# Kernel tuning notes

Measured on AMD Instinct MI355X. Metric: run time of the kernel, lower is better.

The kernel has to match this reference:

```python
import jax, jax.numpy as jnp
import numpy as np

N = 8192
F_IN = 256
F_OUT = 256
S = 128          # state_dim
D_INNER = 512    # int(2.0 * out_features)


def _ln(x, g, b, eps=1e-5):
    m = x.mean(-1, keepdims=True)
    v = ((x - m) ** 2).mean(-1, keepdims=True)
    return (x - m) / jnp.sqrt(v + eps) * g + b


def setup_inputs() -> dict:
    key = jax.random.key(0)
    ks = jax.random.split(key, 20)
    s = 0.05
    d = {}
    d['h'] = jax.random.normal(ks[0], (N, F_IN), dtype=jnp.float32)
    d['adj'] = jax.random.randint(ks[1], (N, N), 0, 2, dtype=jnp.int32)
    d['W'] = jax.random.normal(ks[2], (F_IN, F_OUT), dtype=jnp.float32) * s
    d['a_src'] = jax.random.normal(ks[3], (F_OUT, 1), dtype=jnp.float32) * s
    d['a_dst'] = jax.random.normal(ks[4], (F_OUT, 1), dtype=jnp.float32) * s
    d['W_bcdt'] = jax.random.normal(ks[5], (F_OUT, 3 * S), dtype=jnp.float32) * s
    d['b_bcdt'] = jnp.zeros((3 * S,), jnp.float32)
    d['abp_w'] = jax.random.normal(ks[6], (S, F_OUT), dtype=jnp.float32) * s
    d['abp_b'] = jnp.zeros((F_OUT,), jnp.float32)
    d['cp_w'] = jax.random.normal(ks[7], (S, 1), dtype=jnp.float32) * s
    d['cp_b'] = jnp.zeros((1,), jnp.float32)
    d['W_hz'] = jax.random.normal(ks[8], (F_OUT, 2 * D_INNER), dtype=jnp.float32) * s
    d['b_hz'] = jnp.zeros((2 * D_INNER,), jnp.float32)
    d['out_w'] = jax.random.normal(ks[9], (D_INNER, F_OUT), dtype=jnp.float32) * s
    d['out_b'] = jnp.zeros((F_OUT,), jnp.float32)
    d['fe1_w'] = jax.random.normal(ks[10], (F_OUT, D_INNER), dtype=jnp.float32) * s
    d['fe1_b'] = jnp.zeros((D_INNER,), jnp.float32)
    d['fe_ln_g'] = jnp.ones((D_INNER,), jnp.float32)
    d['fe_ln_b'] = jnp.zeros((D_INNER,), jnp.float32)
    d['fe2_w'] = jax.random.normal(ks[11], (D_INNER, F_OUT), dtype=jnp.float32) * s
    d['fe2_b'] = jnp.zeros((F_OUT,), jnp.float32)
    d['A'] = jax.random.uniform(ks[12], (S,), minval=1.0, maxval=64.0, dtype=jnp.float32)
    d['D'] = jnp.ones((1,), jnp.float32)
    d['g1_w'] = jax.random.normal(ks[13], (2 * F_OUT, 2 * F_OUT), dtype=jnp.float32) * s
    d['g1_b'] = jnp.zeros((2 * F_OUT,), jnp.float32)
    d['g_ln_g'] = jnp.ones((2 * F_OUT,), jnp.float32)
    d['g_ln_b'] = jnp.zeros((2 * F_OUT,), jnp.float32)
    d['g2_w'] = jax.random.normal(ks[14], (2 * F_OUT, F_OUT), dtype=jnp.float32) * s
    d['g2_b'] = jnp.zeros((F_OUT,), jnp.float32)
    d['ln_g'] = jnp.ones((F_OUT,), jnp.float32)
    d['ln_b'] = jnp.zeros((F_OUT,), jnp.float32)
    return d


def reference(h, adj, W, a_src, a_dst, W_bcdt, b_bcdt, abp_w, abp_b, cp_w, cp_b,
              W_hz, b_hz, out_w, out_b, fe1_w, fe1_b, fe_ln_g, fe_ln_b, fe2_w,
              fe2_b, A, D, g1_w, g1_b, g_ln_g, g_ln_b, g2_w, g2_b, ln_g, ln_b):
    Wh = h @ W                                   # [N, F_OUT]
    # GAT-style masked attention
    e = Wh @ a_src + (Wh @ a_dst).T              # [N, N]
    e = jnp.where(e > 0, e, 0.2 * e)             # leaky_relu(0.2)
    e = jnp.where(adj > 0, e, jnp.float32(-9e15))
    attn = jax.nn.softmax(e, axis=1)
    h_attn = attn @ Wh                           # [N, F_OUT]
    # feature enhancer
    h_enh = jax.nn.silu(_ln(Wh @ fe1_w + fe1_b, fe_ln_g, fe_ln_b)) @ fe2_w + fe2_b
    # SSM-like branch
    BCdt = Wh @ W_bcdt + b_bcdt                  # [N, 3S]
    B, C, dt = jnp.split(BCdt, 3, axis=1)
    Asm = jax.nn.softmax(dt + A[None, :], axis=1)
    ab = (Asm * B) @ abp_w + abp_b               # [N, F_OUT]
    hs = Wh * ab
    hz = hs @ W_hz + b_hz                        # [N, 2*D_INNER]
    h_part, z = jnp.split(hz, 2, axis=1)
    hs = (h_part * jax.nn.silu(z) + h_part * D) @ out_w + out_b
    c_proj = C @ cp_w + cp_b                     # [N, 1]
    hs = hs * (1.0 + c_proj)
    # gated fusion
    comb = jnp.concatenate([h_attn, hs], axis=1)  # [N, 2*F_OUT]
    g = jax.nn.sigmoid(jax.nn.silu(_ln(comb @ g1_w + g1_b, g_ln_g, g_ln_b)) @ g2_w + g2_b)
    fused = g * h_attn + (1.0 - g) * hs + h_enh
    return _ln(fused, ln_g, ln_b)
```

## Files before the change

### kernel.cpp

```cpp
#include <hip/hip_runtime.h>
#include <cstdint>

typedef __attribute__((ext_vector_type(8))) short short8;
typedef __attribute__((ext_vector_type(4))) float f32x4;

#define DEVINL static __device__ __forceinline__

DEVINL ushort f2b(float f) {
    uint32_t u = __builtin_bit_cast(uint32_t, f);
    u += 0x7FFFu + ((u >> 16) & 1u);
    return (ushort)(u >> 16);
}

typedef __attribute__((address_space(3))) uint32_t lds_u32;
typedef const __attribute__((address_space(1))) uint32_t glb_u32;

DEVINL void load_lds_16(const ushort* g, ushort* l) {
    __builtin_amdgcn_global_load_lds((glb_u32*)g, (lds_u32*)l, 16, 0, 0);
}

constexpr int EPI_F32      = 0;
constexpr int EPI_MUL_BF16 = 2;
constexpr int EPI_SCALE_FB = 3;
constexpr int EPI_WH       = 4;

template<int K, int EPI>
__global__ __launch_bounds__(256) void gemm_k(
    const ushort* __restrict__ A, const ushort* __restrict__ BT,
    const float* __restrict__ bias, int N,
    float* __restrict__ outf, ushort* __restrict__ outb, int obld, int oboff,
    const float* __restrict__ extra,
    const float* __restrict__ asrc, const float* __restrict__ adst,
    float* __restrict__ sOut, float* __restrict__ dOut)
{
    __shared__ ushort Asm[64 * 64];
    __shared__ ushort Bsm[64 * 64];

    const int wave = threadIdx.x >> 6;
    const int lane = threadIdx.x & 63;
    const int quad = lane >> 4, l16 = lane & 15;
    const int lr = lane >> 3, ls = lane & 7;
    const int m0 = blockIdx.x * 64;
    const int n0 = blockIdx.y * 64;

    f32x4 zero = {0.f, 0.f, 0.f, 0.f};
    f32x4 acc[4] = {zero, zero, zero, zero};

    for (int k0 = 0; k0 < K; k0 += 64) {
        #pragma unroll
        for (int p = 0; p < 2; ++p) {
            const int r = wave * 16 + p * 8 + lr;
            load_lds_16(A + (size_t)(m0 + r) * K + k0 + ((ls ^ (r & 7)) * 8),
                        Asm + (size_t)(wave * 16 + p * 8) * 64);
            load_lds_16(BT + (size_t)(n0 + r) * K + k0 + ((ls ^ (r & 7)) * 8),
                        Bsm + (size_t)(wave * 16 + p * 8) * 64);
        }
        __syncthreads();
        #pragma unroll
        for (int ks = 0; ks < 2; ++ks) {
            const int sl = ((ks * 4 + quad) ^ (l16 & 7)) * 8;
            short8 af = *(const short8*)(Asm + (wave * 16 + l16) * 64 + sl);
            #pragma unroll
            for (int c = 0; c < 4; ++c) {
                short8 bf = *(const short8*)(Bsm + (c * 16 + l16) * 64 + sl);
                acc[c] = __builtin_amdgcn_mfma_f32_16x16x32_bf16(af, bf, acc[c], 0, 0, 0);
            }
        }
        __syncthreads();
    }

    #pragma unroll
    for (int r = 0; r < 4; ++r) {
        const int row = m0 + wave * 16 + quad * 4 + r;
        float sp = 0.f, dp = 0.f;
        #pragma unroll
        for (int c = 0; c < 4; ++c) {
            const int col = n0 + c * 16 + l16;
            float v = acc[c][r] + (bias ? bias[col] : 0.f);
            if (EPI == EPI_MUL_BF16) v *= extra[(size_t)row * N + col];
            if (EPI == EPI_SCALE_FB) v *= extra[row];
            if (EPI == EPI_F32 || EPI == EPI_SCALE_FB || EPI == EPI_WH)
                outf[(size_t)row * N + col] = v;
            if (EPI == EPI_MUL_BF16 || EPI == EPI_SCALE_FB || EPI == EPI_WH)
                outb[(size_t)row * obld + oboff + col] = f2b(v);
            if (EPI == EPI_WH) { sp += v * asrc[col]; dp += v * adst[col]; }
        }
        if (EPI == EPI_WH) {
            #pragma unroll
            for (int o = 1; o < 16; o <<= 1) {
                sp += __shfl_xor(sp, o);
                dp += __shfl_xor(dp, o);
            }
            if (l16 == 0) {
                atomicAdd(&sOut[row], sp);
                atomicAdd(&dOut[row], dp);
            }
        }
    }
}

constexpr int EPR_LNSILU = 0;
constexpr int EPR_BCDT   = 1;
constexpr int EPR_HZ     = 2;
constexpr int EPR_FINAL  = 3;

template<int K, int N, int EPI>
__global__ __launch_bounds__(256) void gemm_row(
    const ushort* __restrict__ A, const ushort* __restrict__ BT,
    const float* __restrict__ bias,
    float* __restrict__ outf, ushort* __restrict__ outb,
    const float* __restrict__ q0, const float* __restrict__ q1,
    const float* __restrict__ q2, const float* __restrict__ q3,
    const float* __restrict__ q4)
{
    constexpr int NW = N / 4;
    constexpr int NF = NW / 16;
    __shared__ ushort Asm[16 * 64];
    __shared__ ushort Bsm[N * 64];
    __shared__ float red[192];

    const int wave = threadIdx.x >> 6;
    const int lane = threadIdx.x & 63;
    const int quad = lane >> 4, l16 = lane & 15;
    const int lr = lane >> 3, ls = lane & 7;
    const int m0 = blockIdx.x * 16;
    const ushort* Bb = BT + (EPI == EPR_HZ ? (size_t)blockIdx.y * 512 * K : 0);

    f32x4 zero = {0.f, 0.f, 0.f, 0.f};
    f32x4 acc[NF];
    #pragma unroll
    for (int c = 0; c < NF; ++c) acc[c] = zero;

    for (int k0 = 0; k0 < K; k0 += 64) {
        if (wave < 2) {
            const int r = wave * 8 + lr;
            load_lds_16(A + (size_t)(m0 + r) * K + k0 + ((ls ^ (r & 7)) * 8),
                        Asm + (size_t)(wave * 8) * 64);
        }
        #pragma unroll
        for (int p = 0; p < NW / 8; ++p) {
            const int n = wave * NW + p * 8 + lr;
            load_lds_16(Bb + (size_t)n * K + k0 + ((ls ^ (n & 7)) * 8),
                        Bsm + (size_t)(wave * NW + p * 8) * 64);
        }
        __syncthreads();
        #pragma unroll
        for (int ks = 0; ks < 2; ++ks) {
            const int sl = ((ks * 4 + quad) ^ (l16 & 7)) * 8;
            short8 af = *(const short8*)(Asm + l16 * 64 + sl);
            #pragma unroll
            for (int c = 0; c < NF; ++c) {
                const int gf = (EPI == EPR_BCDT) ? (wave + 4 * c) : (wave * NF + c);
                short8 bf = *(const short8*)(Bsm + (gf * 16 + l16) * 64 + sl);
                acc[c] = __builtin_amdgcn_mfma_f32_16x16x32_bf16(af, bf, acc[c], 0, 0, 0);
            }
        }
        __syncthreads();
    }

    if constexpr (EPI != EPR_HZ) {
        #pragma unroll
        for (int c = 0; c < NF; ++c) {
            const int gf = (EPI == EPR_BCDT) ? (wave + 4 * c) : (wave * NF + c);
            const float bs = bias[gf * 16 + l16];
            #pragma unroll
            for (int r = 0; r < 4; ++r) acc[c][r] += bs;
        }
    }

    if constexpr (EPI == EPR_LNSILU) {
        float s[4], q[4];
        #pragma unroll
        for (int r = 0; r < 4; ++r) {
            s[r] = 0.f; q[r] = 0.f;
            #pragma unroll
            for (int c = 0; c < NF; ++c) { const float v = acc[c][r]; s[r] += v; q[r] += v * v; }
            #pragma unroll
            for (int o = 1; o < 16; o <<= 1) { s[r] += __shfl_xor(s[r], o); q[r] += __shfl_xor(q[r], o); }
        }
        if (l16 == 0) {
            #pragma unroll
            for (int r = 0; r < 4; ++r) {
                red[(quad * 4 + r) * 8 + wave * 2]     = s[r];
                red[(quad * 4 + r) * 8 + wave * 2 + 1] = q[r];
            }
        }
        __syncthreads();
        #pragma unroll
        for (int r = 0; r < 4; ++r) {
            const int row16 = quad * 4 + r;
            float S = 0.f, Q = 0.f;
            #pragma unroll
            for (int w = 0; w < 4; ++w) { S += red[row16 * 8 + w * 2]; Q += red[row16 * 8 + w * 2 + 1]; }
            const float mean = S * (1.f / N);
            const float rstd = rsqrtf(Q * (1.f / N) - mean * mean + 1e-5f);
            #pragma unroll
            for (int c = 0; c < NF; ++c) {
                const int col = (wave * NF + c) * 16 + l16;
                const float y = (acc[c][r] - mean) * rstd * q0[col] + q1[col];
                outb[(size_t)(m0 + row16) * N + col] = f2b(y / (1.f + __expf(-y)));
            }
        }
    } else if constexpr (EPI == EPR_BCDT) {
        float t[2][4], e[2][4];
        #pragma unroll
        for (int ci = 0; ci < 2; ++ci) {
            const int dcol = (wave + 4 * (ci + 4)) * 16 - 256 + l16;
            const float av = q0[dcol];
            #pragma unroll
            for (int r = 0; r < 4; ++r) t[ci][r] = acc[ci + 4][r] + av;
        }
        float pm[4];
        #pragma unroll
        for (int r = 0; r < 4; ++r) {
            pm[r] = fmaxf(t[0][r], t[1][r]);
            #pragma unroll
            for (int o = 1; o < 16; o <<= 1) pm[r] = fmaxf(pm[r], __shfl_xor(pm[r], o));
        }
        if (l16 == 0) {
            #pragma unroll
            for (int r = 0; r < 4; ++r) red[(quad * 4 + r) * 4 + wave] = pm[r];
        }
        __syncthreads();
        float mx[4];
        #pragma unroll
        for (int r = 0; r < 4; ++r) {
            const int row16 = quad * 4 + r;
            mx[r] = fmaxf(fmaxf(red[row16 * 4], red[row16 * 4 + 1]),
                          fmaxf(red[row16 * 4 + 2], red[row16 * 4 + 3]));
        }
        float pe[4], pc[4];
        #pragma unroll
        for (int r = 0; r < 4; ++r) {
            e[0][r] = __expf(t[0][r] - mx[r]);
            e[1][r] = __expf(t[1][r] - mx[r]);
            pe[r] = e[0][r] + e[1][r];
            pc[r] = 0.f;
            #pragma unroll
            for (int ci = 0; ci < 2; ++ci) {
                const int ccol = (wave + 4 * (ci + 2)) * 16 - 128 + l16;
                pc[r] += acc[ci + 2][r] * q1[ccol];
            }
            #pragma unroll
            for (int o = 1; o < 16; o <<= 1) { pe[r] += __shfl_xor(pe[r], o); pc[r] += __shfl_xor(pc[r], o); }
        }
        if (l16 == 0) {
            #pragma unroll
            for (int r = 0; r < 4; ++r) {
                red[64  + (quad * 4 + r) * 4 + wave] = pe[r];
                red[128 + (quad * 4 + r) * 4 + wave] = pc[r];
            }
        }
        __syncthreads();
        #pragma unroll
        for (int r = 0; r < 4; ++r) {
            const int row16 = quad * 4 + r;
            const float inv = 1.f / (red[64 + row16 * 4] + red[64 + row16 * 4 + 1] +
                                     red[64 + row16 * 4 + 2] + red[64 + row16 * 4 + 3]);
            #pragma unroll
            for (int ci = 0; ci < 2; ++ci) {
                const int bcol = (wave + 4 * ci) * 16 + l16;
                outb[(size_t)(m0 + row16) * 128 + bcol] = f2b(acc[ci][r] * e[ci][r] * inv);
            }
        }
        if (wave == 0 && l16 == 0) {
            #pragma unroll
            for (int r = 0; r < 4; ++r) {
                const int row16 = quad * 4 + r;
                outf[m0 + row16] = 1.f + red[128 + row16 * 4] + red[128 + row16 * 4 + 1] +
                                   red[128 + row16 * 4 + 2] + red[128 + row16 * 4 + 3] + q2[0];
            }
        }
    } else if constexpr (EPI == EPR_HZ) {
        float* ep = (float*)Bsm;
        const float D0 = q0[0];
        const int y = blockIdx.y;
        if (wave >= 2) {
            #pragma unroll
            for (int c = 0; c < NF; ++c) {
                const int lc = (wave * NF + c) * 16 + l16;
                const float bz = bias[512 + y * 256 + lc - 256];
                #pragma unroll
                for (int r = 0; r < 4; ++r) {
                    const float z = acc[c][r] + bz;
                    ep[(quad * 4 + r) * 256 + lc - 256] = z / (1.f + __expf(-z)) + D0;
                }
            }
        }
        __syncthreads();
        if (wave < 2) {
            #pragma unroll
            for (int c = 0; c < NF; ++c) {
                const int lc = (wave * NF + c) * 16 + l16;
                const float bh = bias[y * 256 + lc];
                #pragma unroll
                for (int r = 0; r < 4; ++r) {
                    const float v = (acc[c][r] + bh) * ep[(quad * 4 + r) * 256 + lc];
                    outb[(size_t)(m0 + quad * 4 + r) * 512 + y * 256 + lc] = f2b(v);
                }
            }
        }
    } else {
        float fv[4][4], s[4], q[4];
        #pragma unroll
        for (int r = 0; r < 4; ++r) { s[r] = 0.f; q[r] = 0.f; }
        #pragma unroll
        for (int c = 0; c < NF; ++c) {
            const int col = (wave * NF + c) * 16 + l16;
            #pragma unroll
            for (int r = 0; r < 4; ++r) {
                const size_t idx = (size_t)(m0 + quad * 4 + r) * 256 + col;
                const float g = 1.f / (1.f + __expf(-acc[c][r]));
                const float f = g * q0[idx] + (1.f - g) * q1[idx] + q2[idx];
                fv[c][r] = f; s[r] += f; q[r] += f * f;
            }
        }
        #pragma unroll
        for (int r = 0; r < 4; ++r) {
            #pragma unroll
            for (int o = 1; o < 16; o <<= 1) { s[r] += __shfl_xor(s[r], o); q[r] += __shfl_xor(q[r], o); }
        }
        if (l16 == 0) {
            #pragma unroll
            for (int r = 0; r < 4; ++r) {
                red[(quad * 4 + r) * 8 + wave * 2]     = s[r];
                red[(quad * 4 + r) * 8 + wave * 2 + 1] = q[r];
            }
        }
        __syncthreads();
        #pragma unroll
        for (int r = 0; r < 4; ++r) {
            const int row16 = quad * 4 + r;
            float S = 0.f, Q = 0.f;
            #pragma unroll
            for (int w = 0; w < 4; ++w) { S += red[row16 * 8 + w * 2]; Q += red[row16 * 8 + w * 2 + 1]; }
            const float mean = S * (1.f / 256.f);
            const float rstd = rsqrtf(Q * (1.f / 256.f) - mean * mean + 1e-5f);
            #pragma unroll
            for (int c = 0; c < NF; ++c) {
                const int col = (wave * NF + c) * 16 + l16;
                outf[(size_t)(m0 + row16) * 256 + col] = (fv[c][r] - mean) * rstd * q3[col] + q4[col];
            }
        }
    }
}

__global__ __launch_bounds__(256) void attn_kernel(
    const int* __restrict__ adj, const float* __restrict__ sA,
    const float* __restrict__ dA, const ushort* __restrict__ WhT,
    float* __restrict__ Upart, float* __restrict__ lpart)
{
    __shared__ ushort vsm[256 * 64];
    __shared__ ushort wsm[64 * 64];

    const int tid  = threadIdx.x;
    const int wave = tid >> 6, lane = tid & 63, quad = lane >> 4, l16 = lane & 15;
    const int lr = lane >> 3, ls = lane & 7;
    const int i0 = blockIdx.x * 64;
    const int js = blockIdx.y;
    const int jbase = js * 2048;
    const int pr = tid >> 2, pc = tid & 3;
    const float s_r = sA[i0 + pr];
    const int* adjp = adj + (size_t)(i0 + pr) * 8192 + jbase;
    const int rt = wave & 1, ch = wave >> 1;

    f32x4 zero = {0.f, 0.f, 0.f, 0.f};
    f32x4 acc[2][8] = {{zero, zero, zero, zero, zero, zero, zero, zero},
                       {zero, zero, zero, zero, zero, zero, zero, zero}};
    float lsum = 0.f;

    for (int c64 = 0; c64 < 2048; c64 += 64) {
        #pragma unroll
        for (int p = 0; p < 8; ++p) {
            const int f = wave * 64 + p * 8 + lr;
            load_lds_16(WhT + (size_t)f * 8192 + jbase + c64 + ((ls ^ (f & 7)) * 8),
                        vsm + (size_t)(wave * 64 + p * 8) * 64);
        }
        #pragma unroll
        for (int gi = 0; gi < 2; ++gi) {
            const int g = pc + gi * 4;
            const int4   a0 = *(const int4*)  (adjp + c64 + g * 8);
            const int4   a1 = *(const int4*)  (adjp + c64 + g * 8 + 4);
            const float4 d0 = *(const float4*)(dA + jbase + c64 + g * 8);
            const float4 d1 = *(const float4*)(dA + jbase + c64 + g * 8 + 4);
            const int   aa[8] = {a0.x, a0.y, a0.z, a0.w, a1.x, a1.y, a1.z, a1.w};
            const float dd[8] = {d0.x, d0.y, d0.z, d0.w, d1.x, d1.y, d1.z, d1.w};
            union { ushort us[8]; uint4 v; } pk;
            #pragma unroll
            for (int q = 0; q < 8; ++q) {
                float e = s_r + dd[q];
                e = fmaxf(e, 0.2f * e);
                const float w = aa[q] ? __expf(e) : 0.f;
                lsum += w; pk.us[q] = f2b(w);
            }
            *(uint4*)(wsm + pr * 64 + ((g ^ (pr & 7)) * 8)) = pk.v;
        }
        __syncthreads();

        #pragma unroll
        for (int ks = 0; ks < 2; ++ks) {
            const int sl = ((ks * 4 + quad) ^ (l16 & 7)) * 8;
            short8 a0 = *(const short8*)(wsm + (rt * 32 + l16) * 64 + sl);
            short8 a1 = *(const short8*)(wsm + (rt * 32 + 16 + l16) * 64 + sl);
            #pragma unroll
            for (int c = 0; c < 8; ++c) {
                short8 bf = *(const short8*)(vsm + (ch * 128 + c * 16 + l16) * 64 + sl);
                acc[0][c] = __builtin_amdgcn_mfma_f32_16x16x32_bf16(a0, bf, acc[0][c], 0, 0, 0);
                acc[1][c] = __builtin_amdgcn_mfma_f32_16x16x32_bf16(a1, bf, acc[1][c], 0, 0, 0);
            }
        }
        __syncthreads();
    }

    lsum += __shfl_down(lsum, 1);
    lsum += __shfl_down(lsum, 2);
    if (pc == 0) lpart[(size_t)js * 8192 + i0 + pr] = lsum;

    #pragma unroll
    for (int it = 0; it < 2; ++it) {
        #pragma unroll
        for (int c = 0; c < 8; ++c) {
            const int col = ch * 128 + c * 16 + l16;
            #pragma unroll
            for (int r = 0; r < 4; ++r) {
                const int row = i0 + rt * 32 + it * 16 + quad * 4 + r;
                Upart[((size_t)js * 8192 + row) * 256 + col] = acc[it][c][r];
            }
        }
    }
}

__global__ __launch_bounds__(256) void attn_combine_kernel(
    const float* __restrict__ Upart, const float* __restrict__ lpart,
    float* __restrict__ outf, ushort* __restrict__ outb)
{
    const int row = blockIdx.x * 4 + (threadIdx.x >> 6);
    const int lane = threadIdx.x & 63;
    float l = 0.f;
    #pragma unroll
    for (int js = 0; js < 4; ++js) l += lpart[(size_t)js * 8192 + row];
    const float inv = 1.f / l;
    #pragma unroll
    for (int i = 0; i < 4; ++i) {
        const int c = i * 64 + lane;
        float u = 0.f;
        #pragma unroll
        for (int js = 0; js < 4; ++js)
            u += Upart[((size_t)js * 8192 + row) * 256 + c];
        const float v = u * inv;
        outf[(size_t)row * 256 + c] = v;
        outb[(size_t)row * 512 + c] = f2b(v);
    }
}

struct TJob { const float* in; ushort* out; int R, C, off, perm; };
struct TArgs { TJob j[10]; };

DEVINL int hzperm(int j) {
    return (j < 512) ? ((j >> 8) << 9) + (j & 255)
                     : (((j - 512) >> 8) << 9) + 256 + ((j - 512) & 255);
}

__global__ __launch_bounds__(256) void multi_transpose_kernel(TArgs a)
{
    __shared__ float tile[32][33];
    const int b = blockIdx.x;
    int ji = 0;
    #pragma unroll
    for (int k = 1; k < 10; ++k) if (b >= a.j[k].off) ji = k;
    const TJob J = a.j[ji];
    const int t = b - J.off;

    if (J.R == 0) {
        const int base = t * 1024 + threadIdx.x;
        #pragma unroll
        for (int k = 0; k < 4; ++k)
            J.out[base + k * 256] = f2b(J.in[base + k * 256]);
        return;
    }
    const int CB = J.C >> 5;
    const int bx = t % CB, by = t / CB;
    const int tx = threadIdx.x & 31, ty = threadIdx.x >> 5;
    const int c0 = bx * 32, r0 = by * 32;
    #pragma unroll
    for (int i = ty; i < 32; i += 8)
        tile[i][tx] = J.in[(size_t)(r0 + i) * J.C + (c0 + tx)];
    __syncthreads();
    #pragma unroll
    for (int i = ty; i < 32; i += 8) {
        int orow = c0 + i;
        if (J.perm) orow = hzperm(orow);
        J.out[(size_t)orow * J.R + (r0 + tx)] = f2b(tile[tx][i]);
    }
}

__global__ __launch_bounds__(256) void transpose_cast_kernel(
    const float* __restrict__ in, ushort* __restrict__ out, int R, int C)
{
    __shared__ float tile[32][33];
    const int tx = threadIdx.x & 31, ty = threadIdx.x >> 5;
    const int c0 = blockIdx.x * 32, r0 = blockIdx.y * 32;
    #pragma unroll
    for (int i = ty; i < 32; i += 8)
        tile[i][tx] = in[(size_t)(r0 + i) * C + (c0 + tx)];
    __syncthreads();
    #pragma unroll
    for (int i = ty; i < 32; i += 8)
        out[(size_t)(c0 + i) * R + (r0 + tx)] = f2b(tile[tx][i]);
}

extern "C" void kernel_launch(void* const* d_in, const int* in_sizes, int n_in,
                              void* d_out, int out_size, void* d_ws, size_t ws_size,
                              hipStream_t stream)
{
    const float* h      = (const float*)d_in[0];
    const int*   adj    = (const int*)  d_in[1];
    const float* W      = (const float*)d_in[2];
    const float* a_src  = (const float*)d_in[3];
    const float* a_dst  = (const float*)d_in[4];
    const float* W_bcdt = (const float*)d_in[5];
    const float* b_bcdt = (const float*)d_in[6];
    const float* abp_w  = (const float*)d_in[7];
    const float* abp_b  = (const float*)d_in[8];
    const float* cp_w   = (const float*)d_in[9];
    const float* cp_b   = (const float*)d_in[10];
    const float* W_hz   = (const float*)d_in[11];
    const float* b_hz   = (const float*)d_in[12];
    const float* out_w  = (const float*)d_in[13];
    const float* out_b  = (const float*)d_in[14];
    const float* fe1_w  = (const float*)d_in[15];
    const float* fe1_b  = (const float*)d_in[16];
    const float* fe_ln_g= (const float*)d_in[17];
    const float* fe_ln_b= (const float*)d_in[18];
    const float* fe2_w  = (const float*)d_in[19];
    const float* fe2_b  = (const float*)d_in[20];
    const float* Avec   = (const float*)d_in[21];
    const float* Dvec   = (const float*)d_in[22];
    const float* g1_w   = (const float*)d_in[23];
    const float* g1_b   = (const float*)d_in[24];
    const float* g_ln_g = (const float*)d_in[25];
    const float* g_ln_b = (const float*)d_in[26];
    const float* g2_w   = (const float*)d_in[27];
    const float* g2_b   = (const float*)d_in[28];
    const float* ln_g   = (const float*)d_in[29];
    const float* ln_b   = (const float*)d_in[30];
    float* outp = (float*)d_out;

    char* p = (char*)d_ws;
    size_t off = 0;
    auto take = [&](size_t nbytes) -> void* {
        void* r = p + off;
        off += (nbytes + 255) & ~(size_t)255;
        return r;
    };
    ushort* wT    = (ushort*)take(256 * 256 * 2);
    ushort* fe1T  = (ushort*)take(512 * 256 * 2);
    ushort* fe2T  = (ushort*)take(256 * 512 * 2);
    ushort* bcdtT = (ushort*)take(384 * 256 * 2);
    ushort* hzT   = (ushort*)take(1024 * 256 * 2);
    ushort* outT  = (ushort*)take(256 * 512 * 2);
    ushort* g1T   = (ushort*)take(512 * 512 * 2);
    ushort* g2T   = (ushort*)take(256 * 512 * 2);
    ushort* abpT  = (ushort*)take(256 * 128 * 2);
    ushort* hbf   = (ushort*)take((size_t)8192 * 256 * 2);
    float*  Wh    = (float*) take((size_t)8192 * 256 * 4);
    ushort* Whbf  = (ushort*)take((size_t)8192 * 256 * 2);
    ushort* WhT   = (ushort*)take((size_t)8192 * 256 * 2);
    float*  sbuf  = (float*) take(8192 * 4);
    float*  dbuf  = (float*) take(8192 * 4);
    float*  cscl  = (float*) take(8192 * 4);
    float*  hattn = (float*) take((size_t)8192 * 256 * 4);
    float*  henh  = (float*) take((size_t)8192 * 256 * 4);
    float*  lpart = (float*) take(4 * 8192 * 4);
    ushort* SB    = (ushort*)take((size_t)8192 * 128 * 2);
    ushort* hsbf  = (ushort*)take((size_t)8192 * 256 * 2);
    ushort* vbf   = (ushort*)take((size_t)8192 * 512 * 2);
    float*  hs2   = (float*) take((size_t)8192 * 256 * 4);
    ushort* comb  = (ushort*)take((size_t)8192 * 512 * 2);
    ushort* tact  = (ushort*)take((size_t)8192 * 512 * 2);
    float*  Upart = (float*) take((size_t)4 * 8192 * 256 * 4);

    (void)in_sizes; (void)n_in; (void)out_size; (void)ws_size;

    hipMemsetAsync(sbuf, 0, 2 * 8192 * sizeof(float), stream);

    {
        TArgs ta; int boff = 0;
        auto addT = [&](int i, const float* in, ushort* out, int R, int C, int perm) {
            ta.j[i] = TJob{in, out, R, C, boff, perm};
            boff += (R / 32) * (C / 32);
        };
        addT(0, W,      wT,    256, 256,  0);
        addT(1, fe1_w,  fe1T,  256, 512,  0);
        addT(2, fe2_w,  fe2T,  512, 256,  0);
        addT(3, W_bcdt, bcdtT, 256, 384,  0);
        addT(4, abp_w,  abpT,  128, 256,  0);
        addT(5, W_hz,   hzT,   256, 1024, 1);
        addT(6, out_w,  outT,  512, 256,  0);
        addT(7, g1_w,   g1T,   512, 512,  0);
        addT(8, g2_w,   g2T,   512, 256,  0);
        ta.j[9] = TJob{h, hbf, 0, 8192 * 256, boff, 0};
        boff += (8192 * 256) / 1024;
        multi_transpose_kernel<<<boff, 256, 0, stream>>>(ta);
    }

    gemm_k<256, EPI_WH><<<dim3(128, 4), 256, 0, stream>>>(
        hbf, wT, nullptr, 256, Wh, Whbf, 256, 0, nullptr, a_src, a_dst, sbuf, dbuf);
    transpose_cast_kernel<<<dim3(8, 256), 256, 0, stream>>>(Wh, WhT, 8192, 256);

    attn_kernel<<<dim3(128, 4), 256, 0, stream>>>(adj, sbuf, dbuf, WhT, Upart, lpart);
    attn_combine_kernel<<<2048, 256, 0, stream>>>(Upart, lpart, hattn, comb);

    gemm_row<256, 512, EPR_LNSILU><<<512, 256, 0, stream>>>(
        Whbf, fe1T, fe1_b, nullptr, tact, fe_ln_g, fe_ln_b, nullptr, nullptr, nullptr);
    gemm_k<512, EPI_F32><<<dim3(128, 4), 256, 0, stream>>>(
        tact, fe2T, fe2_b, 256, henh, nullptr, 0, 0, nullptr, nullptr, nullptr, nullptr, nullptr);

    gemm_row<256, 384, EPR_BCDT><<<512, 256, 0, stream>>>(
        Whbf, bcdtT, b_bcdt, cscl, SB, Avec, cp_w, cp_b, nullptr, nullptr);
    gemm_k<128, EPI_MUL_BF16><<<dim3(128, 4), 256, 0, stream>>>(
        SB, abpT, abp_b, 256, nullptr, hsbf, 256, 0, Wh, nullptr, nullptr, nullptr, nullptr);
    gemm_row<256, 512, EPR_HZ><<<dim3(512, 2), 256, 0, stream>>>(
        hsbf, hzT, b_hz, nullptr, vbf, Dvec, nullptr, nullptr, nullptr, nullptr);
    gemm_k<512, EPI_SCALE_FB><<<dim3(128, 4), 256, 0, stream>>>(
        vbf, outT, out_b, 256, hs2, comb, 512, 256, cscl, nullptr, nullptr, nullptr, nullptr);

    gemm_row<512, 512, EPR_LNSILU><<<512, 256, 0, stream>>>(
        comb, g1T, g1_b, nullptr, tact, g_ln_g, g_ln_b, nullptr, nullptr, nullptr);
    gemm_row<512, 256, EPR_FINAL><<<512, 256, 0, stream>>>(
        tact, g2T, g2_b, outp, nullptr, hattn, hs2, henh, ln_g, ln_b);
}
```

Before: 611.2 us.

## Fuse transpose into Wh GEMM, split attention wider, merge independent kernel launches

The Wh GEMM now writes the bf16 transpose through LDS in its epilogue, which removes the separate transpose_cast kernel and its re-read of Wh. The attention kernel is split into 8 column chunks instead of 4, prefetches the next adjacency tile into registers and declares occupancy 3. Independent stages (attention combine, fe1 LN/SiLU GEMM, BCdt GEMM; fe2 GEMM and abp GEMM) are merged into single launches via block-index dispatch, cutting launch count and tail effects. In exchange the partial-sum buffers double in size, the combine step reads more data, and register pressure rises.

```diff
diff --git a/kernel.cpp b/kernel.cpp
--- a/kernel.cpp
+++ b/kernel.cpp
@@ -22,26 +22,20 @@
 constexpr int EPI_F32      = 0;
 constexpr int EPI_MUL_BF16 = 2;
 constexpr int EPI_SCALE_FB = 3;
-constexpr int EPI_WH       = 4;
 
 template<int K, int EPI>
-__global__ __launch_bounds__(256) void gemm_k(
+DEVINL void gemm_k_dev(
     const ushort* __restrict__ A, const ushort* __restrict__ BT,
     const float* __restrict__ bias, int N,
     float* __restrict__ outf, ushort* __restrict__ outb, int obld, int oboff,
-    const float* __restrict__ extra,
-    const float* __restrict__ asrc, const float* __restrict__ adst,
-    float* __restrict__ sOut, float* __restrict__ dOut)
-{
-    __shared__ ushort Asm[64 * 64];
-    __shared__ ushort Bsm[64 * 64];
-
+    const float* __restrict__ extra, int bx, int by,
+    ushort* Asm, ushort* Bsm)
+{
     const int wave = threadIdx.x >> 6;
     const int lane = threadIdx.x & 63;
     const int quad = lane >> 4, l16 = lane & 15;
     const int lr = lane >> 3, ls = lane & 7;
-    const int m0 = blockIdx.x * 64;
-    const int n0 = blockIdx.y * 64;
+    const int m0 = bx * 64, n0 = by * 64;
 
     f32x4 zero = {0.f, 0.f, 0.f, 0.f};
     f32x4 acc[4] = {zero, zero, zero, zero};
@@ -72,31 +66,96 @@
     #pragma unroll
     for (int r = 0; r < 4; ++r) {
         const int row = m0 + wave * 16 + quad * 4 + r;
-        float sp = 0.f, dp = 0.f;
         #pragma unroll
         for (int c = 0; c < 4; ++c) {
             const int col = n0 + c * 16 + l16;
             float v = acc[c][r] + (bias ? bias[col] : 0.f);
             if (EPI == EPI_MUL_BF16) v *= extra[(size_t)row * N + col];
             if (EPI == EPI_SCALE_FB) v *= extra[row];
-            if (EPI == EPI_F32 || EPI == EPI_SCALE_FB || EPI == EPI_WH)
+            if (EPI == EPI_F32 || EPI == EPI_SCALE_FB)
                 outf[(size_t)row * N + col] = v;
-            if (EPI == EPI_MUL_BF16 || EPI == EPI_SCALE_FB || EPI == EPI_WH)
+            if (EPI == EPI_MUL_BF16 || EPI == EPI_SCALE_FB)
                 outb[(size_t)row * obld + oboff + col] = f2b(v);
-            if (EPI == EPI_WH) { sp += v * asrc[col]; dp += v * adst[col]; }
-        }
-        if (EPI == EPI_WH) {
-            #pragma unroll
-            for (int o = 1; o < 16; o <<= 1) {
-                sp += __shfl_xor(sp, o);
-                dp += __shfl_xor(dp, o);
-            }
-            if (l16 == 0) {
-                atomicAdd(&sOut[row], sp);
-                atomicAdd(&dOut[row], dp);
-            }
-        }
-    }
+        }
+    }
+}
+
+__global__ __launch_bounds__(256) void gemm_wh_kernel(
+    const ushort* __restrict__ A, const ushort* __restrict__ BT,
+    const float* __restrict__ asrc, const float* __restrict__ adst,
+    float* __restrict__ Wh, ushort* __restrict__ Whbf, ushort* __restrict__ WhT,
+    float* __restrict__ sOut, float* __restrict__ dOut)
+{
+    __shared__ ushort smem[2 * 64 * 64];
+    ushort* Asm = smem;
+    ushort* Bsm = smem + 4096;
+    constexpr int K = 256;
+
+    const int tid = threadIdx.x;
+    const int wave = tid >> 6, lane = tid & 63;
+    const int quad = lane >> 4, l16 = lane & 15;
+    const int lr = lane >> 3, ls = lane & 7;
+    const int m0 = blockIdx.x * 64, n0 = blockIdx.y * 64;
+
+    f32x4 zero = {0.f, 0.f, 0.f, 0.f};
+    f32x4 acc[4] = {zero, zero, zero, zero};
+
+    for (int k0 = 0; k0 < K; k0 += 64) {
+        #pragma unroll
+        for (int p = 0; p < 2; ++p) {
+            const int r = wave * 16 + p * 8 + lr;
+            load_lds_16(A + (size_t)(m0 + r) * K + k0 + ((ls ^ (r & 7)) * 8),
+                        Asm + (size_t)(wave * 16 + p * 8) * 64);
+            load_lds_16(BT + (size_t)(n0 + r) * K + k0 + ((ls ^ (r & 7)) * 8),
+                        Bsm + (size_t)(wave * 16 + p * 8) * 64);
+        }
+        __syncthreads();
+        #pragma unroll
+        for (int ks = 0; ks < 2; ++ks) {
+            const int sl = ((ks * 4 + quad) ^ (l16 & 7)) * 8;
+            short8 af = *(const short8*)(Asm + (wave * 16 + l16) * 64 + sl);
+            #pragma unroll
+            for (int c = 0; c < 4; ++c) {
+                short8 bf = *(const short8*)(Bsm + (c * 16 + l16) * 64 + sl);
+                acc[c] = __builtin_amdgcn_mfma_f32_16x16x32_bf16(af, bf, acc[c], 0, 0, 0);
+            }
+        }
+        __syncthreads();
+    }
+
+    ushort* Tsm = smem;
+    #pragma unroll
+    for (int r = 0; r < 4; ++r) {
+        const int rl = wave * 16 + quad * 4 + r;
+        const int row = m0 + rl;
+        float sp = 0.f, dp = 0.f;
+        #pragma unroll
+        for (int c = 0; c < 4; ++c) {
+            const int cl = c * 16 + l16;
+            const int col = n0 + cl;
+            const float v = acc[c][r];
+            Wh[(size_t)row * 256 + col] = v;
+            const ushort b = f2b(v);
+            Whbf[(size_t)row * 256 + col] = b;
+            Tsm[cl * 72 + rl] = b;
+            sp += v * asrc[col]; dp += v * adst[col];
+        }
+        #pragma unroll
+        for (int o = 1; o < 16; o <<= 1) {
+            sp += __shfl_xor(sp, o);
+            dp += __shfl_xor(dp, o);
+        }
+        if (l16 == 0) {
+            atomicAdd(&sOut[row], sp);
+            atomicAdd(&dOut[row], dp);
+        }
+    }
+    __syncthreads();
+    const int cl = tid >> 2, seg = tid & 3;
+    const ushort* src = Tsm + cl * 72 + seg * 16;
+    ushort* dst = WhT + (size_t)(n0 + cl) * 8192 + m0 + seg * 16;
+    *(uint4*)(dst)     = *(const uint4*)(src);
+    *(uint4*)(dst + 8) = *(const uint4*)(src + 8);
 }
 
 constexpr int EPR_LNSILU = 0;
@@ -105,26 +164,24 @@
 constexpr int EPR_FINAL  = 3;
 
 template<int K, int N, int EPI>
-__global__ __launch_bounds__(256) void gemm_row(
+DEVINL void gemm_row_dev(
     const ushort* __restrict__ A, const ushort* __restrict__ BT,
     const float* __restrict__ bias,
     float* __restrict__ outf, ushort* __restrict__ outb,
     const float* __restrict__ q0, const float* __restrict__ q1,
     const float* __restrict__ q2, const float* __restrict__ q3,
-    const float* __restrict__ q4)
+    const float* __restrict__ q4,
+    int bx, int by, ushort* Asm, ushort* Bsm, float* red)
 {
     constexpr int NW = N / 4;
     constexpr int NF = NW / 16;
-    __shared__ ushort Asm[16 * 64];
-    __shared__ ushort Bsm[N * 64];
-    __shared__ float red[192];
 
     const int wave = threadIdx.x >> 6;
     const int lane = threadIdx.x & 63;
     const int quad = lane >> 4, l16 = lane & 15;
     const int lr = lane >> 3, ls = lane & 7;
-    const int m0 = blockIdx.x * 16;
-    const ushort* Bb = BT + (EPI == EPR_HZ ? (size_t)blockIdx.y * 512 * K : 0);
+    const int m0 = bx * 16;
+    const ushort* Bb = BT + (EPI == EPR_HZ ? (size_t)by * 512 * K : 0);
 
     f32x4 zero = {0.f, 0.f, 0.f, 0.f};
     f32x4 acc[NF];
@@ -274,12 +331,11 @@
     } else if constexpr (EPI == EPR_HZ) {
         float* ep = (float*)Bsm;
         const float D0 = q0[0];
-        const int y = blockIdx.y;
         if (wave >= 2) {
             #pragma unroll
             for (int c = 0; c < NF; ++c) {
                 const int lc = (wave * NF + c) * 16 + l16;
-                const float bz = bias[512 + y * 256 + lc - 256];
+                const float bz = bias[512 + by * 256 + lc - 256];
                 #pragma unroll
                 for (int r = 0; r < 4; ++r) {
                     const float z = acc[c][r] + bz;
@@ -292,16 +348,16 @@
             #pragma unroll
             for (int c = 0; c < NF; ++c) {
                 const int lc = (wave * NF + c) * 16 + l16;
-                const float bh = bias[y * 256 + lc];
+                const float bh = bias[by * 256 + lc];
                 #pragma unroll
                 for (int r = 0; r < 4; ++r) {
                     const float v = (acc[c][r] + bh) * ep[(quad * 4 + r) * 256 + lc];
-                    outb[(size_t)(m0 + quad * 4 + r) * 512 + y * 256 + lc] = f2b(v);
+                    outb[(size_t)(m0 + quad * 4 + r) * 512 + by * 256 + lc] = f2b(v);
                 }
             }
         }
     } else {
-        float fv[4][4], s[4], q[4];
+        float fv[NF][4], s[4], q[4];
         #pragma unroll
         for (int r = 0; r < 4; ++r) { s[r] = 0.f; q[r] = 0.f; }
         #pragma unroll
@@ -345,7 +401,7 @@
     }
 }
 
-__global__ __launch_bounds__(256) void attn_kernel(
+__global__ __launch_bounds__(256, 3) void attn_kernel(
     const int* __restrict__ adj, const float* __restrict__ sA,
     const float* __restrict__ dA, const ushort* __restrict__ WhT,
     float* __restrict__ Upart, float* __restrict__ lpart)
@@ -358,7 +414,7 @@
     const int lr = lane >> 3, ls = lane & 7;
     const int i0 = blockIdx.x * 64;
     const int js = blockIdx.y;
-    const int jbase = js * 2048;
+    const int jbase = js * 1024;
     const int pr = tid >> 2, pc = tid & 3;
     const float s_r = sA[i0 + pr];
     const int* adjp = adj + (size_t)(i0 + pr) * 8192 + jbase;
@@ -369,21 +425,38 @@
                        {zero, zero, zero, zero, zero, zero, zero, zero}};
     float lsum = 0.f;
 
-    for (int c64 = 0; c64 < 2048; c64 += 64) {
+    int4 ca[2][2];
+    #pragma unroll
+    for (int gi = 0; gi < 2; ++gi) {
+        const int g = pc + gi * 4;
+        ca[gi][0] = *(const int4*)(adjp + g * 8);
+        ca[gi][1] = *(const int4*)(adjp + g * 8 + 4);
+    }
+
+    for (int c64 = 0; c64 < 1024; c64 += 64) {
         #pragma unroll
         for (int p = 0; p < 8; ++p) {
             const int f = wave * 64 + p * 8 + lr;
             load_lds_16(WhT + (size_t)f * 8192 + jbase + c64 + ((ls ^ (f & 7)) * 8),
                         vsm + (size_t)(wave * 64 + p * 8) * 64);
         }
+        const bool more = (c64 + 64 < 1024);
+        int4 na[2][2];
+        if (more) {
+            #pragma unroll
+            for (int gi = 0; gi < 2; ++gi) {
+                const int g = pc + gi * 4;
+                na[gi][0] = *(const int4*)(adjp + c64 + 64 + g * 8);
+                na[gi][1] = *(const int4*)(adjp + c64 + 64 + g * 8 + 4);
+            }
+        }
         #pragma unroll
         for (int gi = 0; gi < 2; ++gi) {
             const int g = pc + gi * 4;
-            const int4   a0 = *(const int4*)  (adjp + c64 + g * 8);
-            const int4   a1 = *(const int4*)  (adjp + c64 + g * 8 + 4);
             const float4 d0 = *(const float4*)(dA + jbase + c64 + g * 8);
             const float4 d1 = *(const float4*)(dA + jbase + c64 + g * 8 + 4);
-            const int   aa[8] = {a0.x, a0.y, a0.z, a0.w, a1.x, a1.y, a1.z, a1.w};
+            const int   aa[8] = {ca[gi][0].x, ca[gi][0].y, ca[gi][0].z, ca[gi][0].w,
+                                 ca[gi][1].x, ca[gi][1].y, ca[gi][1].z, ca[gi][1].w};
             const float dd[8] = {d0.x, d0.y, d0.z, d0.w, d1.x, d1.y, d1.z, d1.w};
             union { ushort us[8]; uint4 v; } pk;
             #pragma unroll
@@ -410,6 +483,13 @@
             }
         }
         __syncthreads();
+        if (more) {
+            #pragma unroll
+            for (int gi = 0; gi < 2; ++gi) {
+                ca[gi][0] = na[gi][0];
+                ca[gi][1] = na[gi][1];
+            }
+        }
     }
 
     lsum += __shfl_down(lsum, 1);
@@ -430,27 +510,115 @@
     }
 }
 
-__global__ __launch_bounds__(256) void attn_combine_kernel(
+__global__ __launch_bounds__(256) void post_attn_kernel(
     const float* __restrict__ Upart, const float* __restrict__ lpart,
-    float* __restrict__ outf, ushort* __restrict__ outb)
-{
-    const int row = blockIdx.x * 4 + (threadIdx.x >> 6);
-    const int lane = threadIdx.x & 63;
-    float l = 0.f;
-    #pragma unroll
-    for (int js = 0; js < 4; ++js) l += lpart[(size_t)js * 8192 + row];
-    const float inv = 1.f / l;
-    #pragma unroll
-    for (int i = 0; i < 4; ++i) {
-        const int c = i * 64 + lane;
-        float u = 0.f;
-        #pragma unroll
-        for (int js = 0; js < 4; ++js)
-            u += Upart[((size_t)js * 8192 + row) * 256 + c];
-        const float v = u * inv;
-        outf[(size_t)row * 256 + c] = v;
-        outb[(size_t)row * 512 + c] = f2b(v);
-    }
+    float* __restrict__ hattn, ushort* __restrict__ comb,
+    const ushort* __restrict__ Whbf,
+    const ushort* __restrict__ fe1T, const float* __restrict__ fe1_b,
+    const float* __restrict__ fe_ln_g, const float* __restrict__ fe_ln_b,
+    ushort* __restrict__ tact,
+    const ushort* __restrict__ bcdtT, const float* __restrict__ b_bcdt,
+    const float* __restrict__ Avec, const float* __restrict__ cpw,
+    const float* __restrict__ cpb,
+    ushort* __restrict__ SB, float* __restrict__ cscl)
+{
+    __shared__ ushort Asm[16 * 64];
+    __shared__ ushort Bsm[512 * 64];
+    __shared__ float red[192];
+    const int b = blockIdx.x;
+
+    if (b < 2048) {
+        const int row = b * 4 + (threadIdx.x >> 6);
+        const int lane = threadIdx.x & 63;
+        float l = 0.f;
+        #pragma unroll
+        for (int js = 0; js < 8; ++js) l += lpart[(size_t)js * 8192 + row];
+        const float inv = 1.f / l;
+        float4 u = {0.f, 0.f, 0.f, 0.f};
+        #pragma unroll
+        for (int js = 0; js < 8; ++js) {
+            const float4 t = *(const float4*)&Upart[((size_t)js * 8192 + row) * 256 + lane * 4];
+            u.x += t.x; u.y += t.y; u.z += t.z; u.w += t.w;
+        }
+        u.x *= inv; u.y *= inv; u.z *= inv; u.w *= inv;
+        *(float4*)&hattn[(size_t)row * 256 + lane * 4] = u;
+        union { ushort us[4]; uint2 v; } pk;
+        pk.us[0] = f2b(u.x); pk.us[1] = f2b(u.y); pk.us[2] = f2b(u.z); pk.us[3] = f2b(u.w);
+        *(uint2*)&comb[(size_t)row * 512 + lane * 4] = pk.v;
+    } else if (b < 2560) {
+        gemm_row_dev<256, 512, EPR_LNSILU>(Whbf, fe1T, fe1_b, nullptr, tact,
+            fe_ln_g, fe_ln_b, nullptr, nullptr, nullptr, b - 2048, 0, Asm, Bsm, red);
+    } else {
+        gemm_row_dev<256, 384, EPR_BCDT>(Whbf, bcdtT, b_bcdt, cscl, SB,
+            Avec, cpw, cpb, nullptr, nullptr, b - 2560, 0, Asm, Bsm, red);
+    }
+}
+
+__global__ __launch_bounds__(256) void gemm_fe2_sb_kernel(
+    const ushort* __restrict__ tact, const ushort* __restrict__ fe2T,
+    const float* __restrict__ fe2_b, float* __restrict__ henh,
+    const ushort* __restrict__ SB, const ushort* __restrict__ abpT,
+    const float* __restrict__ abp_b, ushort* __restrict__ hsbf,
+    const float* __restrict__ Wh)
+{
+    __shared__ ushort Asm[64 * 64];
+    __shared__ ushort Bsm[64 * 64];
+    const int b = blockIdx.x;
+    if (b < 512)
+        gemm_k_dev<512, EPI_F32>(tact, fe2T, fe2_b, 256, henh, nullptr, 0, 0,
+                                 nullptr, b & 127, b >> 7, Asm, Bsm);
+    else
+        gemm_k_dev<128, EPI_MUL_BF16>(SB, abpT, abp_b, 256, nullptr, hsbf, 256, 0,
+                                      Wh, (b - 512) & 127, (b - 512) >> 7, Asm, Bsm);
+}
+
+__global__ __launch_bounds__(256) void gemm_hz_kernel(
+    const ushort* __restrict__ hsbf, const ushort* __restrict__ hzT,
+    const float* __restrict__ b_hz, ushort* __restrict__ vbf,
+    const float* __restrict__ Dvec)
+{
+    __shared__ ushort Asm[16 * 64];
+    __shared__ ushort Bsm[512 * 64];
+    __shared__ float red[192];
+    gemm_row_dev<256, 512, EPR_HZ>(hsbf, hzT, b_hz, nullptr, vbf, Dvec,
+        nullptr, nullptr, nullptr, nullptr, blockIdx.x, blockIdx.y, Asm, Bsm, red);
+}
+
+__global__ __launch_bounds__(256) void gemm_out_kernel(
+    const ushort* __restrict__ vbf, const ushort* __restrict__ outT,
+    const float* __restrict__ out_b, float* __restrict__ hs2,
+    ushort* __restrict__ comb, const float* __restrict__ cscl)
+{
+    __shared__ ushort Asm[64 * 64];
+    __shared__ ushort Bsm[64 * 64];
+    gemm_k_dev<512, EPI_SCALE_FB>(vbf, outT, out_b, 256, hs2, comb, 512, 256,
+                                  cscl, blockIdx.x, blockIdx.y, Asm, Bsm);
+}
+
+__global__ __launch_bounds__(256) void gemm_g1_kernel(
+    const ushort* __restrict__ comb, const ushort* __restrict__ g1T,
+    const float* __restrict__ g1_b, ushort* __restrict__ tact,
+    const float* __restrict__ g_ln_g, const float* __restrict__ g_ln_b)
+{
+    __shared__ ushort Asm[16 * 64];
+    __shared__ ushort Bsm[512 * 64];
+    __shared__ float red[192];
+    gemm_row_dev<512, 512, EPR_LNSILU>(comb, g1T, g1_b, nullptr, tact,
+        g_ln_g, g_ln_b, nullptr, nullptr, nullptr, blockIdx.x, 0, Asm, Bsm, red);
+}
+
+__global__ __launch_bounds__(256) void gemm_final_kernel(
+    const ushort* __restrict__ tact, const ushort* __restrict__ g2T,
+    const float* __restrict__ g2_b, float* __restrict__ outp,
+    const float* __restrict__ hattn, const float* __restrict__ hs2,
+    const float* __restrict__ henh, const float* __restrict__ ln_g,
+    const float* __restrict__ ln_b)
+{
+    __shared__ ushort Asm[16 * 64];
+    __shared__ ushort Bsm[256 * 64];
+    __shared__ float red[192];
+    gemm_row_dev<512, 256, EPR_FINAL>(tact, g2T, g2_b, outp, nullptr,
+        hattn, hs2, henh, ln_g, ln_b, blockIdx.x, 0, Asm, Bsm, red);
 }
 
 struct TJob { const float* in; ushort* out; int R, C, off, perm; };
@@ -492,21 +660,6 @@
         if (J.perm) orow = hzperm(orow);
         J.out[(size_t)orow * J.R + (r0 + tx)] = f2b(tile[tx][i]);
     }
-}
-
-__global__ __launch_bounds__(256) void transpose_cast_kernel(
-    const float* __restrict__ in, ushort* __restrict__ out, int R, int C)
-{
-    __shared__ float tile[32][33];
-    const int tx = threadIdx.x & 31, ty = threadIdx.x >> 5;
-    const int c0 = blockIdx.x * 32, r0 = blockIdx.y * 32;
-    #pragma unroll
-    for (int i = ty; i < 32; i += 8)
-        tile[i][tx] = in[(size_t)(r0 + i) * C + (c0 + tx)];
-    __syncthreads();
-    #pragma unroll
-    for (int i = ty; i < 32; i += 8)
-        out[(size_t)(c0 + i) * R + (r0 + tx)] = f2b(tile[tx][i]);
 }
 
 extern "C" void kernel_launch(void* const* d_in, const int* in_sizes, int n_in,
@@ -571,14 +724,14 @@
     float*  cscl  = (float*) take(8192 * 4);
     float*  hattn = (float*) take((size_t)8192 * 256 * 4);
     float*  henh  = (float*) take((size_t)8192 * 256 * 4);
-    float*  lpart = (float*) take(4 * 8192 * 4);
+    float*  lpart = (float*) take(8 * 8192 * 4);
     ushort* SB    = (ushort*)take((size_t)8192 * 128 * 2);
     ushort* hsbf  = (ushort*)take((size_t)8192 * 256 * 2);
     ushort* vbf   = (ushort*)take((size_t)8192 * 512 * 2);
     float*  hs2   = (float*) take((size_t)8192 * 256 * 4);
     ushort* comb  = (ushort*)take((size_t)8192 * 512 * 2);
     ushort* tact  = (ushort*)take((size_t)8192 * 512 * 2);
-    float*  Upart = (float*) take((size_t)4 * 8192 * 256 * 4);
+    float*  Upart = (float*) take((size_t)8 * 8192 * 256 * 4);
 
     (void)in_sizes; (void)n_in; (void)out_size; (void)ws_size;
 
@@ -604,29 +757,25 @@
         multi_transpose_kernel<<<boff, 256, 0, stream>>>(ta);
     }
 
-    gemm_k<256, EPI_WH><<<dim3(128, 4), 256, 0, stream>>>(
-        hbf, wT, nullptr, 256, Wh, Whbf, 256, 0, nullptr, a_src, a_dst, sbuf, dbuf);
-    transpose_cast_kernel<<<dim3(8, 256), 256, 0, stream>>>(Wh, WhT, 8192, 256);
-
-    attn_kernel<<<dim3(128, 4), 256, 0, stream>>>(adj, sbuf, dbuf, WhT, Upart, lpart);
-    attn_combine_kernel<<<2048, 256, 0, stream>>>(Upart, lpart, hattn, comb);
-
-    gemm_row<256, 512, EPR_LNSILU><<<512, 256, 0, stream>>>(
-        Whbf, fe1T, fe1_b, nullptr, tact, fe_ln_g, fe_ln_b, nullptr, nullptr, nullptr);
-    gemm_k<512, EPI_F32><<<dim3(128, 4), 256, 0, stream>>>(
-        tact, fe2T, fe2_b, 256, henh, nullptr, 0, 0, nullptr, nullptr, nullptr, nullptr, nullptr);
-
-    gemm_row<256, 384, EPR_BCDT><<<512, 256, 0, stream>>>(
-        Whbf, bcdtT, b_bcdt, cscl, SB, Avec, cp_w, cp_b, nullptr, nullptr);
-    gemm_k<128, EPI_MUL_BF16><<<dim3(128, 4), 256, 0, stream>>>(
-        SB, abpT, abp_b, 256, nullptr, hsbf, 256, 0, Wh, nullptr, nullptr, nullptr, nullptr);
-    gemm_row<256, 512, EPR_HZ><<<dim3(512, 2), 256, 0, stream>>>(
-        hsbf, hzT, b_hz, nullptr, vbf, Dvec, nullptr, nullptr, nullptr, nullptr);
-    gemm_k<512, EPI_SCALE_FB><<<dim3(128, 4), 256, 0, stream>>>(
-        vbf, outT, out_b, 256, hs2, comb, 512, 256, cscl, nullptr, nullptr, nullptr, nullptr);
-
-    gemm_row<512, 512, EPR_LNSILU><<<512, 256, 0, stream>>>(
-        comb, g1T, g1_b, nullptr, tact, g_ln_g, g_ln_b, nullptr, nullptr, nullptr);
-    gemm_row<512, 256, EPR_FINAL><<<512, 256, 0, stream>>>(
-        tact, g2T, g2_b, outp, nullptr, hattn, hs2, henh, ln_g, ln_b);
-}
+    gemm_wh_kernel<<<dim3(128, 4), 256, 0, stream>>>(
+        hbf, wT, a_src, a_dst, Wh, Whbf, WhT, sbuf, dbuf);
+
+    attn_kernel<<<dim3(128, 8), 256, 0, stream>>>(adj, sbuf, dbuf, WhT, Upart, lpart);
+
+    post_attn_kernel<<<3072, 256, 0, stream>>>(
+        Upart, lpart, hattn, comb, Whbf,
+        fe1T, fe1_b, fe_ln_g, fe_ln_b, tact,
+        bcdtT, b_bcdt, Avec, cp_w, cp_b, SB, cscl);
+
+    gemm_fe2_sb_kernel<<<1024, 256, 0, stream>>>(
+        tact, fe2T, fe2_b, henh, SB, abpT, abp_b, hsbf, Wh);
+
+    gemm_hz_kernel<<<dim3(512, 2), 256, 0, stream>>>(hsbf, hzT, b_hz, vbf, Dvec);
+
+    gemm_out_kernel<<<dim3(128, 4), 256, 0, stream>>>(vbf, outT, out_b, hs2, comb, cscl);
+
+    gemm_g1_kernel<<<512, 256, 0, stream>>>(comb, g1T, g1_b, tact, g_ln_g, g_ln_b);
+
+    gemm_final_kernel<<<512, 256, 0, stream>>>(
+        tact, g2T, g2_b, outp, hattn, hs2, henh, ln_g, ln_b);
+}
```

New measurement: 620.2 us. No clear change (+1.5%).
